# Kernel tuning notes

Hardware: AMD Instinct MI355X
Metric: run time of the kernel (lower is better)

## Reference

```python
import jax, jax.numpy as jnp
import numpy as np

TOP_K = 2  # k in TopKGate


def setup_inputs() -> dict:
    key = jax.random.key(0)
    k1, k2, k3 = jax.random.split(key, 3)
    B, S, H, E = 4, 2048, 1024, 8
    hidden_states = jax.random.normal(k1, (B, S, H), dtype=jnp.float32)
    Wg = jax.random.normal(k2, (H, E), dtype=jnp.float32) * (H ** -0.5)
    We = jax.random.normal(k3, (E, H, H), dtype=jnp.float32) * (H ** -0.5)
    be = jnp.zeros((E, H), dtype=jnp.float32)
    return {"hidden_states": hidden_states, "Wg": Wg, "We": We, "be": be}


def reference(hidden_states, Wg, We, be):
    # hidden_states: [B, S, H]; Wg: [H, E]; We: [E, H, H]; be: [E, H]
    B, S, H = hidden_states.shape
    T = B * S
    x = hidden_states.reshape(T, H)

    # TopKGate: linear gate -> softmax -> top-k -> renormalize combine weights
    probs = jax.nn.softmax(x @ Wg, axis=-1)              # [T, E]
    top_vals, top_idx = jax.lax.top_k(probs, TOP_K)     # [T, K]
    gates = top_vals / jnp.sum(top_vals, axis=-1, keepdims=True)

    # Experts: run each token through each expert Linear, then gather top-k
    expert_out = jnp.einsum('th,ehd->etd', x, We) + be[:, None, :]  # [E, T, H]
    tok = jnp.arange(T)[:, None]                         # [T, 1]
    sel = expert_out[top_idx, tok, :]                    # [T, K, H]

    # Weighted combine over top-k experts
    out = jnp.sum(gates[..., None] * sel, axis=1)        # [T, H]
    return out.reshape(B, S, H)
```

## Files before the change

kernel.cpp:

```cpp
#include <hip/hip_runtime.h>
#include <hip/hip_bf16.h>

#define H 1024
#define NEXP 8
#define T_TOK 8192
#define CAP 8192
#define TM 128
#define TN 128
#define CNTSTRIDE 32

typedef __bf16 bf16x8 __attribute__((ext_vector_type(8)));
typedef __bf16 bf16x4 __attribute__((ext_vector_type(4)));
typedef float f32x4 __attribute__((ext_vector_type(4)));

__device__ __forceinline__ void async16(void* lds, const void* g) {
    __builtin_amdgcn_global_load_lds(
        (const __attribute__((address_space(1))) void*)g,
        (__attribute__((address_space(3))) void*)lds, 16, 0, 0);
}

__global__ __launch_bounds__(256) void moe_transpose(
    const float* __restrict__ We, __bf16* __restrict__ WeT) {
    __shared__ __align__(16) float t[64][65];
    const int tid = threadIdx.x;
    const int tt = blockIdx.x;
    const int e  = tt >> 8;
    const int d0 = ((tt >> 4) & 15) * 64;
    const int h0 = (tt & 15) * 64;
    const int tx = tid & 15;
    const int ty = tid >> 4;
    const float* src = We + ((size_t)e << 20);
    __bf16* dst = WeT + ((size_t)e << 20);
#pragma unroll
    for (int p = 0; p < 4; ++p) {
        const int row = p * 16 + ty;
        const float4 v = *(const float4*)(src + (size_t)(h0 + row) * H + d0 + tx * 4);
        t[row][tx * 4 + 0] = v.x; t[row][tx * 4 + 1] = v.y;
        t[row][tx * 4 + 2] = v.z; t[row][tx * 4 + 3] = v.w;
    }
    __syncthreads();
#pragma unroll
    for (int qq = 0; qq < 2; ++qq) {
        const int q = tid + qq * 256;
        const int drow = q >> 3;
        const int seg  = q & 7;
        bf16x8 o;
#pragma unroll
        for (int i = 0; i < 8; ++i) o[i] = (__bf16)t[seg * 8 + i][drow];
        *(bf16x8*)(dst + (size_t)(d0 + drow) * H + h0 + seg * 8) = o;
    }
}

__global__ __launch_bounds__(256) void moe_route(
    const float* __restrict__ x, const float* __restrict__ Wg,
    __bf16* __restrict__ Xb, int* __restrict__ cnt,
    int* __restrict__ ltok,
    int* __restrict__ tsel, float* __restrict__ tgate) {
    __shared__ int   sE[32];
    __shared__ float sG[32];
    __shared__ int   lcnt[NEXP], lbase[NEXP], lslot[32];
    const int tid  = threadIdx.x;
    const int lane = tid & 63;
    const int wave = tid >> 6;
    const int base = blockIdx.x * 16;

    float4 xv[4][4];
#pragma unroll
    for (int tk = 0; tk < 4; ++tk) {
        const float* xr = x + (size_t)(base + wave * 4 + tk) * H;
#pragma unroll
        for (int c = 0; c < 4; ++c)
            xv[tk][c] = *(const float4*)(xr + c * 256 + lane * 4);
    }

    float a[4][NEXP];
#pragma unroll
    for (int tk = 0; tk < 4; ++tk)
#pragma unroll
        for (int e = 0; e < NEXP; ++e) a[tk][e] = 0.f;

#pragma unroll
    for (int c = 0; c < 4; ++c) {
        const float* wgp = Wg + (size_t)(c * 256 + lane * 4) * NEXP;
        float4 w[8];
#pragma unroll
        for (int r = 0; r < 8; ++r) w[r] = *(const float4*)(wgp + r * 4);
#pragma unroll
        for (int tk = 0; tk < 4; ++tk) {
            const float xc[4] = {xv[tk][c].x, xv[tk][c].y, xv[tk][c].z, xv[tk][c].w};
#pragma unroll
            for (int i = 0; i < 4; ++i) {
                a[tk][0] += xc[i] * w[i * 2].x;     a[tk][1] += xc[i] * w[i * 2].y;
                a[tk][2] += xc[i] * w[i * 2].z;     a[tk][3] += xc[i] * w[i * 2].w;
                a[tk][4] += xc[i] * w[i * 2 + 1].x; a[tk][5] += xc[i] * w[i * 2 + 1].y;
                a[tk][6] += xc[i] * w[i * 2 + 1].z; a[tk][7] += xc[i] * w[i * 2 + 1].w;
            }
        }
    }

#pragma unroll
    for (int tk = 0; tk < 4; ++tk) {
        __bf16* xbr = Xb + (size_t)(base + wave * 4 + tk) * H;
#pragma unroll
        for (int c = 0; c < 4; ++c) {
            bf16x4 xo;
            xo[0] = (__bf16)xv[tk][c].x; xo[1] = (__bf16)xv[tk][c].y;
            xo[2] = (__bf16)xv[tk][c].z; xo[3] = (__bf16)xv[tk][c].w;
            *(bf16x4*)(xbr + c * 256 + lane * 4) = xo;
        }
    }

#pragma unroll
    for (int tk = 0; tk < 4; ++tk) {
        const int tl = wave * 4 + tk;
#pragma unroll
        for (int e = 0; e < NEXP; ++e) {
#pragma unroll
            for (int off = 32; off > 0; off >>= 1)
                a[tk][e] += __shfl_xor(a[tk][e], off, 64);
        }
        int i0 = 0;
#pragma unroll
        for (int e = 1; e < NEXP; ++e) if (a[tk][e] > a[tk][i0]) i0 = e;
        int i1 = (i0 == 0) ? 1 : 0;
#pragma unroll
        for (int e = 0; e < NEXP; ++e) if (e != i0 && a[tk][e] > a[tk][i1]) i1 = e;
        const float ex = __expf(a[tk][i1] - a[tk][i0]);
        const float g0 = 1.f / (1.f + ex);
        const float g1 = ex / (1.f + ex);
        if (lane == 0) {
            sE[tl * 2] = i0; sE[tl * 2 + 1] = i1;
            sG[tl * 2] = g0; sG[tl * 2 + 1] = g1;
        }
    }
    if (tid < NEXP) lcnt[tid] = 0;
    __syncthreads();
    if (tid < 32) lslot[tid] = atomicAdd(&lcnt[sE[tid]], 1);
    __syncthreads();
    if (tid < NEXP) lbase[tid] = lcnt[tid] ? atomicAdd(&cnt[tid * CNTSTRIDE], lcnt[tid]) : 0;
    __syncthreads();
    if (tid < 32) {
        const int e = sE[tid];
        const int s = lbase[e] + lslot[tid];
        const int t = base + (tid >> 1);
        ltok[e * CAP + s] = t;
        tsel[t * 2 + (tid & 1)]  = e * CAP + s;
        tgate[t * 2 + (tid & 1)] = sG[tid];
    }
}

__global__ __launch_bounds__(256) void moe_gemm(
    const __bf16* __restrict__ Xb, const __bf16* __restrict__ WeT,
    const float* __restrict__ be, const int* __restrict__ cnt,
    const int* __restrict__ ltok,
    __bf16* __restrict__ Eout) {
    const int e  = blockIdx.x & 7;
    const int nt = (blockIdx.x >> 3) & 7;
    const int mt = blockIdx.x >> 6;
    const int ne = cnt[e * CNTSTRIDE];
    const int m0 = mt * TM;
    if (m0 >= ne) return;
    const int n0 = nt * TN;
    int off = 0;
    for (int i2 = 0; i2 < e; ++i2) off += cnt[i2 * CNTSTRIDE];

    __shared__ __align__(16) __bf16 smem[4 * 4096];
    __bf16* Al  = smem;
    __bf16* Al2 = smem + 4096;
    __bf16* Bl  = smem + 8192;
    __bf16* Bl2 = smem + 12288;
    __shared__ int tokL[TM];

    const int tid = threadIdx.x;
    const int lane = tid & 63;
    const int wave = tid >> 6;

    if (tid < TM) {
        const int gi = m0 + tid;
        tokL[tid] = (gi < ne) ? ltok[e * CAP + gi] : 0;
    }
    __syncthreads();

    const __bf16* Bt = WeT + ((size_t)e << 20);
    const int qr = lane >> 4;
    const int rr = lane & 15;
    const int wr = (wave >> 1) * 64;
    const int wc = (wave & 1) * 64;

    f32x4 acc[4][4];
    const f32x4 z = {0.f, 0.f, 0.f, 0.f};
#pragma unroll
    for (int i = 0; i < 4; ++i)
#pragma unroll
        for (int j = 0; j < 4; ++j) acc[i][j] = z;

    const int c0 = tid, c1 = tid + 256;
    const int ar0 = c0 >> 2, ak0 = (((c0 & 3) ^ ((c0 >> 3) & 3)) * 8);
    const int ar1 = c1 >> 2, ak1 = (((c1 & 3) ^ ((c1 >> 3) & 3)) * 8);
    const size_t arow0 = (size_t)tokL[ar0] * H;
    const size_t arow1 = (size_t)tokL[ar1] * H;
    const size_t brow0 = (size_t)(n0 + ar0) * H;
    const size_t brow1 = (size_t)(n0 + ar1) * H;

    for (int k0 = 0; k0 < H; k0 += 64) {
        async16(&Al [c0 * 8], Xb + arow0 + k0 + ak0);
        async16(&Al [c1 * 8], Xb + arow1 + k0 + ak1);
        async16(&Al2[c0 * 8], Xb + arow0 + k0 + 32 + ak0);
        async16(&Al2[c1 * 8], Xb + arow1 + k0 + 32 + ak1);
        async16(&Bl [c0 * 8], Bt + brow0 + k0 + ak0);
        async16(&Bl [c1 * 8], Bt + brow1 + k0 + ak1);
        async16(&Bl2[c0 * 8], Bt + brow0 + k0 + 32 + ak0);
        async16(&Bl2[c1 * 8], Bt + brow1 + k0 + 32 + ak1);
        __syncthreads();
        {
            bf16x8 af[4], bfr[4];
#pragma unroll
            for (int i = 0; i < 4; ++i) {
                const int ra = wr + i * 16 + rr;
                af[i] = *(const bf16x8*)&Al[ra * 32 + ((qr ^ ((ra >> 1) & 3)) * 8)];
            }
#pragma unroll
            for (int j = 0; j < 4; ++j) {
                const int rb = wc + j * 16 + rr;
                bfr[j] = *(const bf16x8*)&Bl[rb * 32 + ((qr ^ ((rb >> 1) & 3)) * 8)];
            }
#pragma unroll
            for (int i = 0; i < 4; ++i)
#pragma unroll
                for (int j = 0; j < 4; ++j)
                    acc[i][j] = __builtin_amdgcn_mfma_f32_16x16x32_bf16(af[i], bfr[j], acc[i][j], 0, 0, 0);
        }
        {
            bf16x8 af[4], bfr[4];
#pragma unroll
            for (int i = 0; i < 4; ++i) {
                const int ra = wr + i * 16 + rr;
                af[i] = *(const bf16x8*)&Al2[ra * 32 + ((qr ^ ((ra >> 1) & 3)) * 8)];
            }
#pragma unroll
            for (int j = 0; j < 4; ++j) {
                const int rb = wc + j * 16 + rr;
                bfr[j] = *(const bf16x8*)&Bl2[rb * 32 + ((qr ^ ((rb >> 1) & 3)) * 8)];
            }
#pragma unroll
            for (int i = 0; i < 4; ++i)
#pragma unroll
                for (int j = 0; j < 4; ++j)
                    acc[i][j] = __builtin_amdgcn_mfma_f32_16x16x32_bf16(af[i], bfr[j], acc[i][j], 0, 0, 0);
        }
        __syncthreads();
    }

    float bev[4];
#pragma unroll
    for (int j = 0; j < 4; ++j) bev[j] = be[e * H + n0 + wc + j * 16 + rr];

    __bf16* Cw = smem + wave * 4096;
#pragma unroll
    for (int i = 0; i < 4; ++i) {
#pragma unroll
        for (int reg = 0; reg < 4; ++reg) {
            const int row = i * 16 + qr * 4 + reg;
            const int key = (row & 7) * 8;
#pragma unroll
            for (int j = 0; j < 4; ++j) {
                const int c = j * 16 + rr;
                Cw[row * 64 + (c ^ key)] = (__bf16)(acc[i][j][reg] + bev[j]);
            }
        }
    }
    const int lrr = lane & 7, lrg = lane >> 3;
#pragma unroll
    for (int p = 0; p < 8; ++p) {
        const int row = p * 8 + lrg;
        const int rglob = m0 + wr + row;
        if (rglob < ne) {
            const int idx8 = ((lrr ^ (row & 7)) * 8);
            const bf16x8 v = *(const bf16x8*)&Cw[row * 64 + idx8];
            *(bf16x8*)(Eout + (size_t)(off + rglob) * H + n0 + wc + lrr * 8) = v;
        }
    }
}

__global__ __launch_bounds__(256) void moe_combine(
    const __bf16* __restrict__ Eout, const int* __restrict__ cnt,
    const int* __restrict__ tsel, const float* __restrict__ tgate,
    float* __restrict__ out) {
    __shared__ int offs[NEXP];
    if (threadIdx.x < NEXP) {
        int o = 0;
        for (int i = 0; i < (int)threadIdx.x; ++i) o += cnt[i * CNTSTRIDE];
        offs[threadIdx.x] = o;
    }
    __syncthreads();
    const int wave = threadIdx.x >> 6, lane = threadIdx.x & 63;
    const int t = blockIdx.x * 4 + wave;
    const int sel0 = tsel[t * 2],  sel1 = tsel[t * 2 + 1];
    const float g0 = tgate[t * 2], g1  = tgate[t * 2 + 1];
    const int e0 = sel0 >> 13, s0 = sel0 & (CAP - 1);
    const int e1 = sel1 >> 13, s1 = sel1 & (CAP - 1);
    const __bf16* r0 = Eout + (size_t)(offs[e0] + s0) * H;
    const __bf16* r1 = Eout + (size_t)(offs[e1] + s1) * H;
    float* orow = out + (size_t)t * H;
#pragma unroll
    for (int c = 0; c < 2; ++c) {
        const int d = c * 512 + lane * 8;
        const bf16x8 a = *(const bf16x8*)(r0 + d);
        const bf16x8 b = *(const bf16x8*)(r1 + d);
        float4 o0, o1;
        o0.x = g0 * (float)a[0] + g1 * (float)b[0];
        o0.y = g0 * (float)a[1] + g1 * (float)b[1];
        o0.z = g0 * (float)a[2] + g1 * (float)b[2];
        o0.w = g0 * (float)a[3] + g1 * (float)b[3];
        o1.x = g0 * (float)a[4] + g1 * (float)b[4];
        o1.y = g0 * (float)a[5] + g1 * (float)b[5];
        o1.z = g0 * (float)a[6] + g1 * (float)b[6];
        o1.w = g0 * (float)a[7] + g1 * (float)b[7];
        *(float4*)(orow + d)     = o0;
        *(float4*)(orow + d + 4) = o1;
    }
}

extern "C" void kernel_launch(void* const* d_in, const int* in_sizes, int n_in,
                              void* d_out, int out_size, void* d_ws, size_t ws_size,
                              hipStream_t stream) {
    const float* x  = (const float*)d_in[0];
    const float* Wg = (const float*)d_in[1];
    const float* We = (const float*)d_in[2];
    const float* be = (const float*)d_in[3];
    float* out = (float*)d_out;

    char* ws = (char*)d_ws;
    __bf16* Xb   = (__bf16*)ws;
    __bf16* WeT  = (__bf16*)(ws + ((size_t)16 << 20));
    __bf16* Eout = (__bf16*)(ws + ((size_t)32 << 20));
    char*   meta = ws + ((size_t)64 << 20);
    int*    cnt  = (int*)meta;
    int*    ltok = (int*)(meta + 1024);
    int*    tsel = (int*)(meta + 1024 + (size_t)NEXP * CAP * 8);
    float*  tgat = (float*)(meta + 1024 + (size_t)NEXP * CAP * 8 + (size_t)T_TOK * 8);

    hipMemsetAsync(cnt, 0, NEXP * CNTSTRIDE * sizeof(int), stream);

    moe_transpose<<<2048, 256, 0, stream>>>(We, WeT);
    moe_route<<<512, 256, 0, stream>>>(x, Wg, Xb, cnt, ltok, tsel, tgat);
    moe_gemm<<<8 * 8 * (T_TOK / TM), 256, 0, stream>>>(Xb, WeT, be, cnt, ltok, Eout);
    moe_combine<<<T_TOK / 4, 256, 0, stream>>>(Eout, cnt, tsel, tgat, out);
}
```

Measured before the change: 200.4 us.

## Fuse gated combine into expert GEMM epilogue via float atomics

Removes the separate combine kernel and the bf16 intermediate expert-output buffer. Each GEMM tile now scales its results by the per-slot gate and atomically adds them into the fp32 output at the token row, which is zeroed by a memset first. This saves the intermediate write and re-read plus one launch. In exchange it issues scalar float atomicAdds with 64-byte-strided per-lane scatter, adds a 32MB memset, and makes the summation order nondeterministic.

```diff
diff --git a/kernel.cpp b/kernel.cpp
--- a/kernel.cpp
+++ b/kernel.cpp
@@ -54,8 +54,7 @@
 __global__ __launch_bounds__(256) void moe_route(
     const float* __restrict__ x, const float* __restrict__ Wg,
     __bf16* __restrict__ Xb, int* __restrict__ cnt,
-    int* __restrict__ ltok,
-    int* __restrict__ tsel, float* __restrict__ tgate) {
+    int* __restrict__ ltok, float* __restrict__ lgate) {
     __shared__ int   sE[32];
     __shared__ float sG[32];
     __shared__ int   lcnt[NEXP], lbase[NEXP], lslot[32];
@@ -142,18 +141,16 @@
     if (tid < 32) {
         const int e = sE[tid];
         const int s = lbase[e] + lslot[tid];
-        const int t = base + (tid >> 1);
-        ltok[e * CAP + s] = t;
-        tsel[t * 2 + (tid & 1)]  = e * CAP + s;
-        tgate[t * 2 + (tid & 1)] = sG[tid];
+        ltok[e * CAP + s]  = base + (tid >> 1);
+        lgate[e * CAP + s] = sG[tid];
     }
 }
 
 __global__ __launch_bounds__(256) void moe_gemm(
     const __bf16* __restrict__ Xb, const __bf16* __restrict__ WeT,
     const float* __restrict__ be, const int* __restrict__ cnt,
-    const int* __restrict__ ltok,
-    __bf16* __restrict__ Eout) {
+    const int* __restrict__ ltok, const float* __restrict__ lgate,
+    float* __restrict__ out) {
     const int e  = blockIdx.x & 7;
     const int nt = (blockIdx.x >> 3) & 7;
     const int mt = blockIdx.x >> 6;
@@ -161,15 +158,14 @@
     const int m0 = mt * TM;
     if (m0 >= ne) return;
     const int n0 = nt * TN;
-    int off = 0;
-    for (int i2 = 0; i2 < e; ++i2) off += cnt[i2 * CNTSTRIDE];
 
     __shared__ __align__(16) __bf16 smem[4 * 4096];
     __bf16* Al  = smem;
     __bf16* Al2 = smem + 4096;
     __bf16* Bl  = smem + 8192;
     __bf16* Bl2 = smem + 12288;
-    __shared__ int tokL[TM];
+    __shared__ int   tokL[TM];
+    __shared__ float gateL[TM];
 
     const int tid = threadIdx.x;
     const int lane = tid & 63;
@@ -177,7 +173,8 @@
 
     if (tid < TM) {
         const int gi = m0 + tid;
-        tokL[tid] = (gi < ne) ? ltok[e * CAP + gi] : 0;
+        tokL[tid]  = (gi < ne) ? ltok[e * CAP + gi] : 0;
+        gateL[tid] = (gi < ne) ? lgate[e * CAP + gi] : 0.f;
     }
     __syncthreads();
 
@@ -255,69 +252,19 @@
 #pragma unroll
     for (int j = 0; j < 4; ++j) bev[j] = be[e * H + n0 + wc + j * 16 + rr];
 
-    __bf16* Cw = smem + wave * 4096;
 #pragma unroll
     for (int i = 0; i < 4; ++i) {
 #pragma unroll
         for (int reg = 0; reg < 4; ++reg) {
-            const int row = i * 16 + qr * 4 + reg;
-            const int key = (row & 7) * 8;
-#pragma unroll
-            for (int j = 0; j < 4; ++j) {
-                const int c = j * 16 + rr;
-                Cw[row * 64 + (c ^ key)] = (__bf16)(acc[i][j][reg] + bev[j]);
-            }
-        }
-    }
-    const int lrr = lane & 7, lrg = lane >> 3;
-#pragma unroll
-    for (int p = 0; p < 8; ++p) {
-        const int row = p * 8 + lrg;
-        const int rglob = m0 + wr + row;
-        if (rglob < ne) {
-            const int idx8 = ((lrr ^ (row & 7)) * 8);
-            const bf16x8 v = *(const bf16x8*)&Cw[row * 64 + idx8];
-            *(bf16x8*)(Eout + (size_t)(off + rglob) * H + n0 + wc + lrr * 8) = v;
-        }
-    }
-}
-
-__global__ __launch_bounds__(256) void moe_combine(
-    const __bf16* __restrict__ Eout, const int* __restrict__ cnt,
-    const int* __restrict__ tsel, const float* __restrict__ tgate,
-    float* __restrict__ out) {
-    __shared__ int offs[NEXP];
-    if (threadIdx.x < NEXP) {
-        int o = 0;
-        for (int i = 0; i < (int)threadIdx.x; ++i) o += cnt[i * CNTSTRIDE];
-        offs[threadIdx.x] = o;
-    }
-    __syncthreads();
-    const int wave = threadIdx.x >> 6, lane = threadIdx.x & 63;
-    const int t = blockIdx.x * 4 + wave;
-    const int sel0 = tsel[t * 2],  sel1 = tsel[t * 2 + 1];
-    const float g0 = tgate[t * 2], g1  = tgate[t * 2 + 1];
-    const int e0 = sel0 >> 13, s0 = sel0 & (CAP - 1);
-    const int e1 = sel1 >> 13, s1 = sel1 & (CAP - 1);
-    const __bf16* r0 = Eout + (size_t)(offs[e0] + s0) * H;
-    const __bf16* r1 = Eout + (size_t)(offs[e1] + s1) * H;
-    float* orow = out + (size_t)t * H;
-#pragma unroll
-    for (int c = 0; c < 2; ++c) {
-        const int d = c * 512 + lane * 8;
-        const bf16x8 a = *(const bf16x8*)(r0 + d);
-        const bf16x8 b = *(const bf16x8*)(r1 + d);
-        float4 o0, o1;
-        o0.x = g0 * (float)a[0] + g1 * (float)b[0];
-        o0.y = g0 * (float)a[1] + g1 * (float)b[1];
-        o0.z = g0 * (float)a[2] + g1 * (float)b[2];
-        o0.w = g0 * (float)a[3] + g1 * (float)b[3];
-        o1.x = g0 * (float)a[4] + g1 * (float)b[4];
-        o1.y = g0 * (float)a[5] + g1 * (float)b[5];
-        o1.z = g0 * (float)a[6] + g1 * (float)b[6];
-        o1.w = g0 * (float)a[7] + g1 * (float)b[7];
-        *(float4*)(orow + d)     = o0;
-        *(float4*)(orow + d + 4) = o1;
+            const int row = wr + i * 16 + qr * 4 + reg;
+            if (m0 + row < ne) {
+                const float g = gateL[row];
+                float* orow = out + (size_t)tokL[row] * H + n0 + wc;
+#pragma unroll
+                for (int j = 0; j < 4; ++j)
+                    atomicAdd(orow + j * 16 + rr, g * (acc[i][j][reg] + bev[j]));
+            }
+        }
     }
 }
 
@@ -333,17 +280,15 @@
     char* ws = (char*)d_ws;
     __bf16* Xb   = (__bf16*)ws;
     __bf16* WeT  = (__bf16*)(ws + ((size_t)16 << 20));
-    __bf16* Eout = (__bf16*)(ws + ((size_t)32 << 20));
     char*   meta = ws + ((size_t)64 << 20);
     int*    cnt  = (int*)meta;
     int*    ltok = (int*)(meta + 1024);
-    int*    tsel = (int*)(meta + 1024 + (size_t)NEXP * CAP * 8);
-    float*  tgat = (float*)(meta + 1024 + (size_t)NEXP * CAP * 8 + (size_t)T_TOK * 8);
+    float*  lgat = (float*)(meta + 1024 + (size_t)NEXP * CAP * 4);
 
     hipMemsetAsync(cnt, 0, NEXP * CNTSTRIDE * sizeof(int), stream);
+    hipMemsetAsync(out, 0, (size_t)T_TOK * H * sizeof(float), stream);
 
     moe_transpose<<<2048, 256, 0, stream>>>(We, WeT);
-    moe_route<<<512, 256, 0, stream>>>(x, Wg, Xb, cnt, ltok, tsel, tgat);
-    moe_gemm<<<8 * 8 * (T_TOK / TM), 256, 0, stream>>>(Xb, WeT, be, cnt, ltok, Eout);
-    moe_combine<<<T_TOK / 4, 256, 0, stream>>>(Eout, cnt, tsel, tgat, out);
-}
+    moe_route<<<512, 256, 0, stream>>>(x, Wg, Xb, cnt, ltok, lgat);
+    moe_gemm<<<8 * 8 * (T_TOK / TM), 256, 0, stream>>>(Xb, WeT, be, cnt, ltok, lgat, out);
+}
```

Result: slower. 231.6 us (+15.5%).
